# Kernel tuning notes

Hardware: AMD Instinct MI355X
Metric: run time of the kernel (lower is better)

## Reference

```python
import jax, jax.numpy as jnp
import numpy as np

# ---------------- static model configuration (mirrors NeuroNN.__init__) -------------
N = 2000
RATIO = 0.8
N_E = int(N * RATIO)
N_I = N - N_E
NMAX = 60          # Euler fixed-point steps (Nmax in Euler2fixedpt)
NAVG = 15          # trailing steps averaged for convergence metric (Navg)
DT = 1e-3
XTOL = 1e-5
XMIN = 1.0
V_THR = 20.0       # spike threshold of Ricciardi transfer fn (V_rest = 0)
SCALING_G = 1.0
W_FF = 30.0
SIG_EXT = 5.0
DEG = jnp.pi / 180.0

_IS_I = jnp.arange(N) >= N_E
PREF = jnp.concatenate([jnp.linspace(0.0, 179.99, N_E), jnp.linspace(0.0, 179.99, N_I)])
T_INV = 1.0 / jnp.where(_IS_I, 0.01 * 0.5, 0.01)          # T_E=0.01, T_I=0.005
TAU = jnp.where(_IS_I, 0.01, 0.01)                          # tau_E = tau_I = 0.01
TAU_REF = jnp.where(_IS_I, 0.001, 0.005)                    # refractory periods
# connection-type gather index: conn[i,j] = 2*(j is I) + (i is I)  -> 0:ee 1:ei 2:ie 3:ii
CONN = 2 * _IS_I[None, :].astype(jnp.int32) + _IS_I[:, None].astype(jnp.int32)
SIGN_COL = jnp.where(_IS_I, -1.0, 1.0)                      # Dale's law: sign by presynaptic column
DIFF = jnp.abs(PREF[:, None] - PREF[None, :])               # |pref_i - pref_j| (deg)

ORIENTATIONS = jnp.arange(12.0) * 15.0                       # [12]
CONTRASTS = jnp.array([0.0, 0.0432773, 0.103411, 0.186966, 0.303066, 0.464386, 0.68854, 1.0])
# circular Gaussian feed-forward drive, [12, N]
_gauss = jnp.exp((jnp.cos(2.0 * DEG * (ORIENTATIONS[:, None] - PREF[None, :])) - 1.0)
                 / (4.0 * (DEG * W_FF) ** 2))
# all 96 conditions flattened: index c*12 + o, shape [96, N]
INPUT_MEAN = (CONTRASTS[:, None, None] * 20.0 * SCALING_G * _gauss[None]).reshape(96, N)

# ------------- Ricciardi transfer function Phi (Sanzeni rational approximation) ------
_A = [0.22757881388024176, 0.77373949685442023, 0.32056016125642045,
      0.32171431660633076, 0.62718906618071668, 0.93524391761244940,
      1.0616084849547165, 0.64290613877355551, 0.14805913578876898]

def f_ricci(x):
    t = -x / (1.0 + x)
    p = jnp.zeros_like(x)
    for c in reversed(_A):      # Horner: a1*t + ... + a9*t^9
        p = p * t + c
    return jnp.log(2.0 * x + 1.0) + p * t

def g_ricci(x):
    z = x / (2.0 + x)
    enum = (3.5441754117462949 * z - 7.0529131065835378 * z**2 - 56.532378057580381 * z**3
            + 279.56761105465944 * z**4 - 520.37554793489681 * z**5
            + 456.58245777026514 * z**6 - 155.73340457809226 * z**7)
    denom = (1.0 - 4.1357968834226053 * z - 7.2984226138266743 * z**2
             + 98.656602235468327 * z**3 - 334.20436223415163 * z**4
             + 601.08633903294185 * z**5 - 599.58577549598340 * z**6
             + 277.18420330693891 * z**7 - 16.445022798669722 * z**8)
    return enum / denom

def Phi(mu, sigma, tau, tau_ref):
    xp = mu / sigma
    xm = (mu - V_THR) / sigma
    pos = xm > 0
    neg = xp <= 0
    mid = (~pos) & (~neg)
    # branch 1: 0 < xm < xp   (guard values keep unselected lanes finite for vjp)
    xps = jnp.where(pos, xp, 2.0)
    xms = jnp.where(pos, xm, 1.0)
    r_pos = 1.0 / (f_ricci(xps) - f_ricci(xms))
    # branch 2: xm <= 0 < xp
    xpm = jnp.where(mid, xp, 1.0)
    nxm = jnp.clip(jnp.where(mid, -xm, 1.0), 0.0, 9.0)
    r_mid = 1.0 / (f_ricci(xpm) + jnp.exp(nxm ** 2) * g_ricci(nxm))
    # branch 3: xm < xp <= 0
    nxp = jnp.clip(jnp.where(neg, -xp, 0.5), 0.0, 9.0)
    nxm2 = jnp.clip(jnp.where(neg, -xm, 1.0), 0.0, 9.0)
    arg = g_ricci(nxm2) - jnp.exp(nxp ** 2 - nxm2 ** 2) * g_ricci(nxp)
    r_neg = jnp.exp(-nxm2 ** 2 - jnp.log(jnp.maximum(arg, 1e-12)))
    r = jnp.where(pos, r_pos, jnp.where(mid, r_mid, r_neg))
    return 1.0 / (tau_ref + tau / jnp.maximum(r, 1e-12))

# --------------------------- weight construction ------------------------------------
def _build_weights(j_param, p_param, w_param, rand_matrix):
    J = jnp.exp(j_param)                         # positive efficacies, [4]
    P = jax.nn.sigmoid(2.0 * jnp.exp(p_param))   # probs in (0,1), steepness-2 sigmoid
    Wd = jnp.exp(w_param)                        # positive widths (deg)
    J_mat = J[CONN]                              # [N, N] gathers by connection type
    P_mat = P[CONN]
    W_mat = Wd[CONN]
    z = jnp.exp((jnp.cos(2.0 * DEG * DIFF) - 1.0) / (4.0 * (DEG * W_mat) ** 2))
    W = SIGN_COL[None, :] * J_mat * jax.nn.sigmoid(32.0 * (P_mat * z - rand_matrix))
    return W, W * W

# ------------------ Euler fixed-point solve, all 96 conditions at once ---------------
def _solve(W, W2):
    sd2 = SIG_EXT ** 2
    def step(r, _):
        mu = TAU * (r @ W.T) + INPUT_MEAN                  # [96, N]
        sig = jnp.sqrt(TAU * (r @ W2.T) + sd2)
        dr = DT * T_INV * (Phi(mu, sig, TAU, TAU_REF) - r)
        r = r + dr
        m = jnp.max(jnp.abs(dr) / jnp.maximum(jnp.abs(r), XMIN), axis=1) / XTOL  # [96]
        return r, m
    r0 = jnp.zeros((96, N), dtype=W.dtype)
    r_fp, ms = jax.lax.scan(step, r0, None, length=NMAX)
    avg_step = jnp.mean(ms[-NAVG:])
    return r_fp, avg_step

def setup_inputs() -> dict:
    key = jax.random.key(0)
    k1, k2, k3, k4 = jax.random.split(key, 4)
    j_param = jnp.log(jnp.array([2.0, 1.5, 3.0, 2.5], dtype=jnp.float32)) + 0.1 * jax.random.normal(k1, (4,), dtype=jnp.float32)
    p_param = jnp.log(jnp.array([0.4, 0.3, 0.5, 0.4], dtype=jnp.float32)) + 0.1 * jax.random.normal(k2, (4,), dtype=jnp.float32)
    w_param = jnp.log(jnp.array([32.0, 32.0, 32.0, 32.0], dtype=jnp.float32)) + 0.1 * jax.random.normal(k3, (4,), dtype=jnp.float32)
    rand_matrix = jax.random.uniform(k4, (N, N), dtype=jnp.float32)
    return {"j_param": j_param, "p_param": p_param, "w_param": w_param, "rand_matrix": rand_matrix}

def reference(j_param, p_param, w_param, rand_matrix):
    W, W2 = _build_weights(j_param, p_param, w_param, rand_matrix)
    r_fp, avg_step = _solve(W, W2)
    # [96, N] -> [8, 12, N] -> [N, contrasts, orientations] (matches permute(2,0,1))
    tuning = r_fp.reshape(8, 12, N).transpose(2, 0, 1)
    return tuning, avg_step
```

## Files before the change

### kernel.cpp

```cpp
#include <hip/hip_runtime.h>
#include <hip/hip_bf16.h>

#define N_NEUR 2000
#define N_E    1600
#define KPAD   2048
#define NCOND  96
#define NSTEP  60
#define NAVG   15
#define NBLK   250
#define RSTEP  (NCOND * KPAD)

#define DEGF   0.017453292519943295f
#define TWO_DEG 0.03490658503988659f

typedef __attribute__((ext_vector_type(8))) short bf16x8;
typedef __attribute__((ext_vector_type(4))) float f32x4;

__device__ __forceinline__ float f_ricci(float x){
    float t = -x / (1.0f + x);
    float p = 0.14805913578876898f;
    p = fmaf(p, t, 0.64290613877355551f);
    p = fmaf(p, t, 1.0616084849547165f);
    p = fmaf(p, t, 0.93524391761244940f);
    p = fmaf(p, t, 0.62718906618071668f);
    p = fmaf(p, t, 0.32171431660633076f);
    p = fmaf(p, t, 0.32056016125642045f);
    p = fmaf(p, t, 0.77373949685442023f);
    p = fmaf(p, t, 0.22757881388024176f);
    return logf(2.0f * x + 1.0f) + p * t;
}

__device__ __forceinline__ float g_ricci(float x){
    float z = x / (2.0f + x);
    float z2 = z * z, z3 = z2 * z, z4 = z2 * z2, z5 = z4 * z, z6 = z3 * z3, z7 = z6 * z, z8 = z4 * z4;
    float en = 3.5441754117462949f * z - 7.0529131065835378f * z2 - 56.532378057580381f * z3
             + 279.56761105465944f * z4 - 520.37554793489681f * z5
             + 456.58245777026514f * z6 - 155.73340457809226f * z7;
    float de = 1.0f - 4.1357968834226053f * z - 7.2984226138266743f * z2
             + 98.656602235468327f * z3 - 334.20436223415163f * z4
             + 601.08633903294185f * z5 - 599.58577549598340f * z6
             + 277.18420330693891f * z7 - 16.445022798669722f * z8;
    return en / de;
}

__device__ __forceinline__ float phi_rate(float mu, float sigma, float tau_ref){
    const float tau = 0.01f;
    float xp = mu / sigma;
    float xm = (mu - 20.0f) / sigma;
    float r;
    if (xm > 0.0f){
        r = 1.0f / (f_ricci(xp) - f_ricci(xm));
    } else if (xp > 0.0f){
        float nxm = fminf(-xm, 9.0f);
        r = 1.0f / (f_ricci(xp) + expf(nxm * nxm) * g_ricci(nxm));
    } else {
        float nxp = fminf(fmaxf(-xp, 0.0f), 9.0f);
        float nxm = fminf(-xm, 9.0f);
        float arg = g_ricci(nxm) - expf(nxp * nxp - nxm * nxm) * g_ricci(nxp);
        r = expf(-nxm * nxm - logf(fmaxf(arg, 1e-12f)));
    }
    return 1.0f / (tau_ref + tau / fmaxf(r, 1e-12f));
}

__device__ __forceinline__ float pref_of(int n){
    return (n < N_E) ? (float)n * (179.99f / 1599.0f)
                     : (float)(n - N_E) * (179.99f / 399.0f);
}

__device__ __forceinline__ unsigned short bf16_rne(float f){
    unsigned int u = __float_as_uint(f);
    u = (u + 0x7fffu + ((u >> 16) & 1u)) >> 16;
    return (unsigned short)u;
}

__device__ __forceinline__ void vmdrain(){
    asm volatile("s_waitcnt vmcnt(0)" ::: "memory");
}

__global__ __launch_bounds__(256) void build_w_kernel(
    const float* __restrict__ jp, const float* __restrict__ pp,
    const float* __restrict__ wp, const float* __restrict__ rnd,
    unsigned short* __restrict__ Wh, unsigned short* __restrict__ Wl,
    unsigned short* __restrict__ W2h)
{
    int e = blockIdx.x * 256 + threadIdx.x;
    int i = e >> 11;
    int j = e & (KPAD - 1);
    float w = 0.0f;
    if (i < N_NEUR && j < N_NEUR){
        int isIi = (i >= N_E) ? 1 : 0;
        int isIj = (j >= N_E) ? 1 : 0;
        int conn = 2 * isIj + isIi;
        float J  = expf(jp[conn]);
        float P  = 1.0f / (1.0f + expf(-2.0f * expf(pp[conn])));
        float Wd = expf(wp[conn]);
        float diff = fabsf(pref_of(i) - pref_of(j));
        float dw = DEGF * Wd;
        float z = expf((cosf(TWO_DEG * diff) - 1.0f) / (4.0f * dw * dw));
        float s = 1.0f / (1.0f + expf(-32.0f * (P * z - rnd[i * N_NEUR + j])));
        float sign = isIj ? -1.0f : 1.0f;
        w = sign * J * s;
    }
    unsigned short hb = bf16_rne(w);
    float hf = __uint_as_float(((unsigned int)hb) << 16);
    Wh[e] = hb;
    Wl[e] = bf16_rne(w - hf);
    W2h[e] = bf16_rne(w * w);
}

__global__ __launch_bounds__(256) void build_im_kernel(float* __restrict__ IM)
{
    int e = blockIdx.x * 256 + threadIdx.x;
    int c = e >> 11;
    int n = e & (KPAD - 1);
    if (n >= N_NEUR){ IM[e] = 0.0f; return; }
    const float contrasts[8] = {0.0f, 0.0432773f, 0.103411f, 0.186966f,
                                0.303066f, 0.464386f, 0.68854f, 1.0f};
    int ci = c / 12;
    int oi = c - ci * 12;
    float orient = (float)oi * 15.0f;
    const float dw = DEGF * 30.0f;
    float g = expf((cosf(TWO_DEG * (orient - pref_of(n))) - 1.0f) / (4.0f * dw * dw));
    IM[e] = contrasts[ci] * 20.0f * g;
}

__global__ __launch_bounds__(512, 2) void solve_kernel(
    const unsigned short* __restrict__ Wh, const unsigned short* __restrict__ Wl,
    const unsigned short* __restrict__ W2h,
    unsigned short* __restrict__ rh, unsigned short* __restrict__ rl,
    unsigned int* __restrict__ flags,
    const float* __restrict__ IM, float* __restrict__ out,
    float* __restrict__ mloc)
{
    __shared__ float red[8][64][25];
    __shared__ float vbuf[48][16];

    const int bid  = blockIdx.x;
    const int tile = bid >> 1;
    const int half = bid & 1;
    const int t  = threadIdx.x;
    const int wv = t >> 6;
    const int ln = t & 63;
    const int nbase = tile * 16;
    const int cbase = half * 48;

    const int lrow = ln & 15;
    const int lk8  = (ln >> 4) * 8;
    const int kw   = wv * 256 + lk8;
    const int nrow = nbase + lrow;

    const unsigned short* pwh = &Wh [nrow * KPAD + kw];
    const unsigned short* pwl = &Wl [nrow * KPAD + kw];
    const unsigned short* pw2 = &W2h[nrow * KPAD + kw];
    bf16x8 wh_f[8], wl_f[8], w2_f[8];
    #pragma unroll
    for (int s = 0; s < 8; ++s){
        wh_f[s] = *reinterpret_cast<const bf16x8*>(pwh + s * 32);
        wl_f[s] = *reinterpret_cast<const bf16x8*>(pwl + s * 32);
        w2_f[s] = *reinterpret_cast<const bf16x8*>(pw2 + s * 32);
    }

    const int wt = wv * 16 + (ln & 15);
    const bool need = (ln < 16) && (wt < 125);
    const unsigned int* fpoll = &flags[((size_t)wt * 2 + half) * 16];

    const int o0 = t, o1 = t + 512;
    const bool has1 = (o1 < 768);
    const int c_l0 = o0 >> 4, n_l0 = o0 & 15;
    const int c_l1 = o1 >> 4, n_l1 = o1 & 15;
    const int m0 = c_l0 >> 4, q0 = c_l0 & 3, lr0 = ((c_l0 & 15) >> 2) * 16 + n_l0;
    const int m1 = c_l1 >> 4, q1 = c_l1 & 3, lr1 = ((c_l1 & 15) >> 2) * 16 + n_l1;
    const int c0 = cbase + c_l0, i0n = nbase + n_l0;
    const int c1 = cbase + c_l1, i1n = nbase + n_l1;
    const float im0 = IM[c0 * KPAD + i0n];
    const float im1 = has1 ? IM[c1 * KPAD + i1n] : 0.0f;
    const bool isI0 = (i0n >= N_E), isI1 = (i1n >= N_E);
    float rf0 = 0.0f, rf1 = 0.0f;

    const int ro0 = (cbase + lrow) * KPAD + kw;

    for (int st = 0; st < NSTEP; ++st){
        if (st > 0){
            const unsigned int* fp = fpoll + (size_t)st * 256 * 16;
            for (;;){
                unsigned int v = need ? __hip_atomic_load(fp, __ATOMIC_RELAXED,
                                                          __HIP_MEMORY_SCOPE_AGENT) : 1u;
                if (__all(v != 0)) break;
                __builtin_amdgcn_s_sleep(1);
            }
        }

        const unsigned short* bhp = rh + (size_t)st * RSTEP + ro0;
        const unsigned short* blp = rl + (size_t)st * RSTEP + ro0;

        f32x4 accm[3], accs[3];
        #pragma unroll
        for (int m = 0; m < 3; ++m){
            accm[m] = (f32x4){0.0f, 0.0f, 0.0f, 0.0f};
            accs[m] = (f32x4){0.0f, 0.0f, 0.0f, 0.0f};
        }

        bf16x8 fh[3][3], fl[3][3];
        #define LOADF(b, s) do {                                                        \
            fh[b][0] = *reinterpret_cast<const bf16x8*>(bhp + (s) * 32            );    \
            fh[b][1] = *reinterpret_cast<const bf16x8*>(bhp + (s) * 32 + 16 * KPAD);    \
            fh[b][2] = *reinterpret_cast<const bf16x8*>(bhp + (s) * 32 + 32 * KPAD);    \
            fl[b][0] = *reinterpret_cast<const bf16x8*>(blp + (s) * 32            );    \
            fl[b][1] = *reinterpret_cast<const bf16x8*>(blp + (s) * 32 + 16 * KPAD);    \
            fl[b][2] = *reinterpret_cast<const bf16x8*>(blp + (s) * 32 + 32 * KPAD);    \
        } while (0)

        LOADF(0, 0);
        LOADF(1, 1);
        #pragma unroll
        for (int s = 0; s < 8; ++s){
            const int cur = s % 3;
            if (s + 2 < 8){ const int nx = (s + 2) % 3; LOADF(nx, s + 2); }
            #pragma unroll
            for (int m = 0; m < 3; ++m){
                accm[m] = __builtin_amdgcn_mfma_f32_16x16x32_bf16(fh[cur][m], wh_f[s], accm[m], 0, 0, 0);
                accm[m] = __builtin_amdgcn_mfma_f32_16x16x32_bf16(fh[cur][m], wl_f[s], accm[m], 0, 0, 0);
                accm[m] = __builtin_amdgcn_mfma_f32_16x16x32_bf16(fl[cur][m], wh_f[s], accm[m], 0, 0, 0);
                accs[m] = __builtin_amdgcn_mfma_f32_16x16x32_bf16(fh[cur][m], w2_f[s], accs[m], 0, 0, 0);
                accs[m] = __builtin_amdgcn_mfma_f32_16x16x32_bf16(fl[cur][m], w2_f[s], accs[m], 0, 0, 0);
            }
        }
        #undef LOADF

        #pragma unroll
        for (int m = 0; m < 3; ++m)
            #pragma unroll
            for (int q = 0; q < 4; ++q){
                red[wv][ln][m * 4 + q]      = accm[m][q];
                red[wv][ln][12 + m * 4 + q] = accs[m][q];
            }
        __syncthreads();

        unsigned short* rho = rh + (size_t)(st + 1) * RSTEP;
        unsigned short* rlo = rl + (size_t)(st + 1) * RSTEP;
        const bool track = (st >= NSTEP - NAVG);

        {
            float ms = 0.0f, ss = 0.0f;
            #pragma unroll
            for (int w = 0; w < 8; ++w){
                ms += red[w][lr0][m0 * 4 + q0];
                ss += red[w][lr0][12 + m0 * 4 + q0];
            }
            const float mu = fmaf(0.01f, ms, im0);
            const float sg = sqrtf(fmaf(0.01f, ss, 25.0f));
            const float rate = phi_rate(mu, sg, isI0 ? 0.001f : 0.005f);
            const float dr = (isI0 ? 0.2f : 0.1f) * (rate - rf0);
            const float rnew = rf0 + dr;
            rf0 = rnew;
            const unsigned short hb = bf16_rne(rnew);
            const float hf = __uint_as_float(((unsigned int)hb) << 16);
            __hip_atomic_store(&rho[c0 * KPAD + i0n], hb,
                               __ATOMIC_RELAXED, __HIP_MEMORY_SCOPE_AGENT);
            __hip_atomic_store(&rlo[c0 * KPAD + i0n], bf16_rne(rnew - hf),
                               __ATOMIC_RELAXED, __HIP_MEMORY_SCOPE_AGENT);
            if (track) vbuf[c_l0][n_l0] = fabsf(dr) / fmaxf(fabsf(rnew), 1.0f);
            if (st == NSTEP - 1) out[i0n * NCOND + c0] = rnew;
        }
        if (has1){
            float ms = 0.0f, ss = 0.0f;
            #pragma unroll
            for (int w = 0; w < 8; ++w){
                ms += red[w][lr1][m1 * 4 + q1];
                ss += red[w][lr1][12 + m1 * 4 + q1];
            }
            const float mu = fmaf(0.01f, ms, im1);
            const float sg = sqrtf(fmaf(0.01f, ss, 25.0f));
            const float rate = phi_rate(mu, sg, isI1 ? 0.001f : 0.005f);
            const float dr = (isI1 ? 0.2f : 0.1f) * (rate - rf1);
            const float rnew = rf1 + dr;
            rf1 = rnew;
            const unsigned short hb = bf16_rne(rnew);
            const float hf = __uint_as_float(((unsigned int)hb) << 16);
            __hip_atomic_store(&rho[c1 * KPAD + i1n], hb,
                               __ATOMIC_RELAXED, __HIP_MEMORY_SCOPE_AGENT);
            __hip_atomic_store(&rlo[c1 * KPAD + i1n], bf16_rne(rnew - hf),
                               __ATOMIC_RELAXED, __HIP_MEMORY_SCOPE_AGENT);
            if (track) vbuf[c_l1][n_l1] = fabsf(dr) / fmaxf(fabsf(rnew), 1.0f);
            if (st == NSTEP - 1) out[i1n * NCOND + c1] = rnew;
        }

        vmdrain();
        __syncthreads();
        if (st < NSTEP - 1 && t == 0)
            __hip_atomic_store(&flags[((size_t)(st + 1) * 256 + tile * 2 + half) * 16], 1u,
                               __ATOMIC_RELAXED, __HIP_MEMORY_SCOPE_AGENT);
        if (track && t < 48){
            float mx = 0.0f;
            #pragma unroll
            for (int j = 0; j < 16; ++j) mx = fmaxf(mx, vbuf[t][j]);
            mloc[((size_t)(st - (NSTEP - NAVG)) * NBLK + bid) * 48 + t] = mx;
        }
    }
}

__global__ __launch_bounds__(128) void finalize_max_kernel(
    const float* __restrict__ mloc, float* __restrict__ m2)
{
    int idx = blockIdx.x * 128 + threadIdx.x;
    if (idx >= NAVG * NCOND) return;
    int st = idx / NCOND, c = idx - st * NCOND;
    int half = c / 48, cl = c - half * 48;
    float mx = 0.0f;
    for (int tile = 0; tile < 125; ++tile)
        mx = fmaxf(mx, mloc[((size_t)st * NBLK + tile * 2 + half) * 48 + cl]);
    m2[idx] = mx;
}

__global__ __launch_bounds__(256) void finalize_sum_kernel(
    const float* __restrict__ m2, float* __restrict__ out)
{
    __shared__ float sbuf[256];
    float s = 0.0f;
    for (int i = threadIdx.x; i < NAVG * NCOND; i += 256) s += m2[i];
    sbuf[threadIdx.x] = s;
    __syncthreads();
    for (int st = 128; st > 0; st >>= 1){
        if (threadIdx.x < st) sbuf[threadIdx.x] += sbuf[threadIdx.x + st];
        __syncthreads();
    }
    if (threadIdx.x == 0)
        out[N_NEUR * NCOND] = sbuf[0] / (float)(NAVG * NCOND) * 1e5f;
}

extern "C" void kernel_launch(void* const* d_in, const int* in_sizes, int n_in,
                              void* d_out, int out_size, void* d_ws, size_t ws_size,
                              hipStream_t stream) {
    const float* jp  = (const float*)d_in[0];
    const float* pp  = (const float*)d_in[1];
    const float* wp  = (const float*)d_in[2];
    const float* rnd = (const float*)d_in[3];
    float* out = (float*)d_out;

    const size_t WELEMS = (size_t)KPAD * KPAD;
    const size_t RBUFS  = (size_t)(NSTEP + 1) * RSTEP;
    unsigned short* Wh  = (unsigned short*)d_ws;
    unsigned short* Wl  = Wh  + WELEMS;
    unsigned short* W2h = Wl  + WELEMS;
    float* IM   = (float*)(W2h + WELEMS);
    float* mloc = IM + (size_t)NCOND * KPAD;
    float* m2   = mloc + (size_t)NAVG * NBLK * 48;
    unsigned short* rh = (unsigned short*)(m2 + NAVG * NCOND);
    unsigned short* rl = rh + RBUFS;
    unsigned int* flags = (unsigned int*)(rl + RBUFS);

    hipMemsetAsync(rh, 0, (size_t)RSTEP * sizeof(unsigned short), stream);
    hipMemsetAsync(rl, 0, (size_t)RSTEP * sizeof(unsigned short), stream);
    hipMemsetAsync(flags, 0, (size_t)(NSTEP + 1) * 256 * 16 * sizeof(unsigned int), stream);

    build_w_kernel<<<(int)(WELEMS / 256), 256, 0, stream>>>(jp, pp, wp, rnd, Wh, Wl, W2h);
    build_im_kernel<<<(int)((NCOND * KPAD) / 256), 256, 0, stream>>>(IM);

    void* args[] = {(void*)&Wh, (void*)&Wl, (void*)&W2h,
                    (void*)&rh, (void*)&rl, (void*)&flags,
                    (void*)&IM, (void*)&out, (void*)&mloc};
    hipLaunchCooperativeKernel((const void*)solve_kernel, dim3(NBLK), dim3(512),
                               args, 0, stream);

    finalize_max_kernel<<<(NAVG * NCOND + 127) / 128, 128, 0, stream>>>(mloc, m2);
    finalize_sum_kernel<<<1, 256, 0, stream>>>(m2, out);
}
```

Measured before the change: 915.5 us.

## Split solver into quarter-condition blocks for twice the workgroups

The fixed-point solver now assigns each block 16 neurons by 24 conditions instead of 48, so it launches 500 blocks with a 4-per-CU launch bound and a normal launch in place of the cooperative one. This is meant to spread the per-step matvec and transfer-function work over more CUs and shorten each step's critical path. The W2 fragment is now reloaded from global every step instead of held in registers, which frees registers but adds traffic. The cross-wave reduction is now two-phase in LDS, and the second MFMA tile covers only 8 real condition rows, so half of it is wasted. The spin-wait now depends on all blocks being resident without a cooperative-launch guarantee.

```diff
diff --git a/kernel.cpp b/kernel.cpp
--- a/kernel.cpp
+++ b/kernel.cpp
@@ -7,7 +7,7 @@
 #define NCOND  96
 #define NSTEP  60
 #define NAVG   15
-#define NBLK   250
+#define NBLK   500
 #define RSTEP  (NCOND * KPAD)
 
 #define DEGF   0.017453292519943295f
@@ -124,7 +124,7 @@
     IM[e] = contrasts[ci] * 20.0f * g;
 }
 
-__global__ __launch_bounds__(512, 2) void solve_kernel(
+__global__ __launch_bounds__(512, 4) void solve_kernel(
     const unsigned short* __restrict__ Wh, const unsigned short* __restrict__ Wl,
     const unsigned short* __restrict__ W2h,
     unsigned short* __restrict__ rh, unsigned short* __restrict__ rl,
@@ -132,17 +132,17 @@
     const float* __restrict__ IM, float* __restrict__ out,
     float* __restrict__ mloc)
 {
-    __shared__ float red[8][64][25];
-    __shared__ float vbuf[48][16];
+    __shared__ float red[4][64][17];
+    __shared__ float vbuf[24][16];
 
     const int bid  = blockIdx.x;
-    const int tile = bid >> 1;
-    const int half = bid & 1;
+    const int tile = bid >> 2;
+    const int qtr  = bid & 3;
     const int t  = threadIdx.x;
     const int wv = t >> 6;
     const int ln = t & 63;
     const int nbase = tile * 16;
-    const int cbase = half * 48;
+    const int cbase = qtr * 24;
 
     const int lrow = ln & 15;
     const int lk8  = (ln >> 4) * 8;
@@ -152,36 +152,37 @@
     const unsigned short* pwh = &Wh [nrow * KPAD + kw];
     const unsigned short* pwl = &Wl [nrow * KPAD + kw];
     const unsigned short* pw2 = &W2h[nrow * KPAD + kw];
-    bf16x8 wh_f[8], wl_f[8], w2_f[8];
+    bf16x8 wh_f[8], wl_f[8];
     #pragma unroll
     for (int s = 0; s < 8; ++s){
         wh_f[s] = *reinterpret_cast<const bf16x8*>(pwh + s * 32);
         wl_f[s] = *reinterpret_cast<const bf16x8*>(pwl + s * 32);
-        w2_f[s] = *reinterpret_cast<const bf16x8*>(pw2 + s * 32);
     }
 
     const int wt = wv * 16 + (ln & 15);
     const bool need = (ln < 16) && (wt < 125);
-    const unsigned int* fpoll = &flags[((size_t)wt * 2 + half) * 16];
-
-    const int o0 = t, o1 = t + 512;
-    const bool has1 = (o1 < 768);
-    const int c_l0 = o0 >> 4, n_l0 = o0 & 15;
-    const int c_l1 = o1 >> 4, n_l1 = o1 & 15;
-    const int m0 = c_l0 >> 4, q0 = c_l0 & 3, lr0 = ((c_l0 & 15) >> 2) * 16 + n_l0;
-    const int m1 = c_l1 >> 4, q1 = c_l1 & 3, lr1 = ((c_l1 & 15) >> 2) * 16 + n_l1;
-    const int c0 = cbase + c_l0, i0n = nbase + n_l0;
-    const int c1 = cbase + c_l1, i1n = nbase + n_l1;
-    const float im0 = IM[c0 * KPAD + i0n];
-    const float im1 = has1 ? IM[c1 * KPAD + i1n] : 0.0f;
-    const bool isI0 = (i0n >= N_E), isI1 = (i1n >= N_E);
-    float rf0 = 0.0f, rf1 = 0.0f;
+    const unsigned int* fpoll = &flags[((size_t)wt * 4 + qtr) * 16];
+
+    const int c_l = t >> 4, n_l = t & 15;
+    const bool act = (t < 384);
+    const int m_e = c_l >> 4;
+    const int rr_e = c_l & 15;
+    const int q_e = rr_e & 3;
+    const int lane_e = ((rr_e >> 2) << 4) + n_l;
+    const int c_g = cbase + c_l;
+    const int i_g = nbase + n_l;
+    const float im = act ? IM[c_g * KPAD + i_g] : 0.0f;
+    const bool isI = (i_g >= N_E);
+    const float tref = isI ? 0.001f : 0.005f;
+    const float gain = isI ? 0.2f : 0.1f;
+    float rfv = 0.0f;
 
     const int ro0 = (cbase + lrow) * KPAD + kw;
+    const int ro1 = (cbase + 16 + (lrow & 7)) * KPAD + kw;
 
     for (int st = 0; st < NSTEP; ++st){
         if (st > 0){
-            const unsigned int* fp = fpoll + (size_t)st * 256 * 16;
+            const unsigned int* fp = fpoll + (size_t)st * NBLK * 16;
             for (;;){
                 unsigned int v = need ? __hip_atomic_load(fp, __ATOMIC_RELAXED,
                                                           __HIP_MEMORY_SCOPE_AGENT) : 1u;
@@ -190,111 +191,92 @@
             }
         }
 
-        const unsigned short* bhp = rh + (size_t)st * RSTEP + ro0;
-        const unsigned short* blp = rl + (size_t)st * RSTEP + ro0;
-
-        f32x4 accm[3], accs[3];
-        #pragma unroll
-        for (int m = 0; m < 3; ++m){
-            accm[m] = (f32x4){0.0f, 0.0f, 0.0f, 0.0f};
-            accs[m] = (f32x4){0.0f, 0.0f, 0.0f, 0.0f};
-        }
-
-        bf16x8 fh[3][3], fl[3][3];
-        #define LOADF(b, s) do {                                                        \
-            fh[b][0] = *reinterpret_cast<const bf16x8*>(bhp + (s) * 32            );    \
-            fh[b][1] = *reinterpret_cast<const bf16x8*>(bhp + (s) * 32 + 16 * KPAD);    \
-            fh[b][2] = *reinterpret_cast<const bf16x8*>(bhp + (s) * 32 + 32 * KPAD);    \
-            fl[b][0] = *reinterpret_cast<const bf16x8*>(blp + (s) * 32            );    \
-            fl[b][1] = *reinterpret_cast<const bf16x8*>(blp + (s) * 32 + 16 * KPAD);    \
-            fl[b][2] = *reinterpret_cast<const bf16x8*>(blp + (s) * 32 + 32 * KPAD);    \
-        } while (0)
-
-        LOADF(0, 0);
-        LOADF(1, 1);
+        const unsigned short* base_h = rh + (size_t)st * RSTEP;
+        const unsigned short* base_l = rl + (size_t)st * RSTEP;
+
+        f32x4 accm[2], accs[2];
+        accm[0] = (f32x4){0.0f, 0.0f, 0.0f, 0.0f};
+        accm[1] = (f32x4){0.0f, 0.0f, 0.0f, 0.0f};
+        accs[0] = (f32x4){0.0f, 0.0f, 0.0f, 0.0f};
+        accs[1] = (f32x4){0.0f, 0.0f, 0.0f, 0.0f};
+
         #pragma unroll
         for (int s = 0; s < 8; ++s){
-            const int cur = s % 3;
-            if (s + 2 < 8){ const int nx = (s + 2) % 3; LOADF(nx, s + 2); }
+            const bf16x8 fh0 = *reinterpret_cast<const bf16x8*>(base_h + ro0 + s * 32);
+            const bf16x8 fh1 = *reinterpret_cast<const bf16x8*>(base_h + ro1 + s * 32);
+            const bf16x8 fl0 = *reinterpret_cast<const bf16x8*>(base_l + ro0 + s * 32);
+            const bf16x8 fl1 = *reinterpret_cast<const bf16x8*>(base_l + ro1 + s * 32);
+            const bf16x8 w2s = *reinterpret_cast<const bf16x8*>(pw2 + s * 32);
+            accm[0] = __builtin_amdgcn_mfma_f32_16x16x32_bf16(fh0, wh_f[s], accm[0], 0, 0, 0);
+            accm[0] = __builtin_amdgcn_mfma_f32_16x16x32_bf16(fh0, wl_f[s], accm[0], 0, 0, 0);
+            accm[0] = __builtin_amdgcn_mfma_f32_16x16x32_bf16(fl0, wh_f[s], accm[0], 0, 0, 0);
+            accs[0] = __builtin_amdgcn_mfma_f32_16x16x32_bf16(fh0, w2s, accs[0], 0, 0, 0);
+            accs[0] = __builtin_amdgcn_mfma_f32_16x16x32_bf16(fl0, w2s, accs[0], 0, 0, 0);
+            accm[1] = __builtin_amdgcn_mfma_f32_16x16x32_bf16(fh1, wh_f[s], accm[1], 0, 0, 0);
+            accm[1] = __builtin_amdgcn_mfma_f32_16x16x32_bf16(fh1, wl_f[s], accm[1], 0, 0, 0);
+            accm[1] = __builtin_amdgcn_mfma_f32_16x16x32_bf16(fl1, wh_f[s], accm[1], 0, 0, 0);
+            accs[1] = __builtin_amdgcn_mfma_f32_16x16x32_bf16(fh1, w2s, accs[1], 0, 0, 0);
+            accs[1] = __builtin_amdgcn_mfma_f32_16x16x32_bf16(fl1, w2s, accs[1], 0, 0, 0);
+        }
+
+        if (wv >= 4){
             #pragma unroll
-            for (int m = 0; m < 3; ++m){
-                accm[m] = __builtin_amdgcn_mfma_f32_16x16x32_bf16(fh[cur][m], wh_f[s], accm[m], 0, 0, 0);
-                accm[m] = __builtin_amdgcn_mfma_f32_16x16x32_bf16(fh[cur][m], wl_f[s], accm[m], 0, 0, 0);
-                accm[m] = __builtin_amdgcn_mfma_f32_16x16x32_bf16(fl[cur][m], wh_f[s], accm[m], 0, 0, 0);
-                accs[m] = __builtin_amdgcn_mfma_f32_16x16x32_bf16(fh[cur][m], w2_f[s], accs[m], 0, 0, 0);
-                accs[m] = __builtin_amdgcn_mfma_f32_16x16x32_bf16(fl[cur][m], w2_f[s], accs[m], 0, 0, 0);
-            }
-        }
-        #undef LOADF
-
-        #pragma unroll
-        for (int m = 0; m < 3; ++m)
+            for (int m = 0; m < 2; ++m)
+                #pragma unroll
+                for (int q = 0; q < 4; ++q){
+                    red[wv - 4][ln][m * 4 + q]     = accm[m][q];
+                    red[wv - 4][ln][8 + m * 4 + q] = accs[m][q];
+                }
+        }
+        __syncthreads();
+        if (wv < 4){
             #pragma unroll
-            for (int q = 0; q < 4; ++q){
-                red[wv][ln][m * 4 + q]      = accm[m][q];
-                red[wv][ln][12 + m * 4 + q] = accs[m][q];
-            }
+            for (int m = 0; m < 2; ++m)
+                #pragma unroll
+                for (int q = 0; q < 4; ++q){
+                    red[wv][ln][m * 4 + q]     += accm[m][q];
+                    red[wv][ln][8 + m * 4 + q] += accs[m][q];
+                }
+        }
         __syncthreads();
 
         unsigned short* rho = rh + (size_t)(st + 1) * RSTEP;
         unsigned short* rlo = rl + (size_t)(st + 1) * RSTEP;
         const bool track = (st >= NSTEP - NAVG);
 
-        {
+        if (act){
             float ms = 0.0f, ss = 0.0f;
             #pragma unroll
-            for (int w = 0; w < 8; ++w){
-                ms += red[w][lr0][m0 * 4 + q0];
-                ss += red[w][lr0][12 + m0 * 4 + q0];
+            for (int w = 0; w < 4; ++w){
+                ms += red[w][lane_e][m_e * 4 + q_e];
+                ss += red[w][lane_e][8 + m_e * 4 + q_e];
             }
-            const float mu = fmaf(0.01f, ms, im0);
+            const float mu = fmaf(0.01f, ms, im);
             const float sg = sqrtf(fmaf(0.01f, ss, 25.0f));
-            const float rate = phi_rate(mu, sg, isI0 ? 0.001f : 0.005f);
-            const float dr = (isI0 ? 0.2f : 0.1f) * (rate - rf0);
-            const float rnew = rf0 + dr;
-            rf0 = rnew;
+            const float rate = phi_rate(mu, sg, tref);
+            const float dr = gain * (rate - rfv);
+            const float rnew = rfv + dr;
+            rfv = rnew;
             const unsigned short hb = bf16_rne(rnew);
             const float hf = __uint_as_float(((unsigned int)hb) << 16);
-            __hip_atomic_store(&rho[c0 * KPAD + i0n], hb,
+            __hip_atomic_store(&rho[c_g * KPAD + i_g], hb,
                                __ATOMIC_RELAXED, __HIP_MEMORY_SCOPE_AGENT);
-            __hip_atomic_store(&rlo[c0 * KPAD + i0n], bf16_rne(rnew - hf),
+            __hip_atomic_store(&rlo[c_g * KPAD + i_g], bf16_rne(rnew - hf),
                                __ATOMIC_RELAXED, __HIP_MEMORY_SCOPE_AGENT);
-            if (track) vbuf[c_l0][n_l0] = fabsf(dr) / fmaxf(fabsf(rnew), 1.0f);
-            if (st == NSTEP - 1) out[i0n * NCOND + c0] = rnew;
-        }
-        if (has1){
-            float ms = 0.0f, ss = 0.0f;
-            #pragma unroll
-            for (int w = 0; w < 8; ++w){
-                ms += red[w][lr1][m1 * 4 + q1];
-                ss += red[w][lr1][12 + m1 * 4 + q1];
-            }
-            const float mu = fmaf(0.01f, ms, im1);
-            const float sg = sqrtf(fmaf(0.01f, ss, 25.0f));
-            const float rate = phi_rate(mu, sg, isI1 ? 0.001f : 0.005f);
-            const float dr = (isI1 ? 0.2f : 0.1f) * (rate - rf1);
-            const float rnew = rf1 + dr;
-            rf1 = rnew;
-            const unsigned short hb = bf16_rne(rnew);
-            const float hf = __uint_as_float(((unsigned int)hb) << 16);
-            __hip_atomic_store(&rho[c1 * KPAD + i1n], hb,
-                               __ATOMIC_RELAXED, __HIP_MEMORY_SCOPE_AGENT);
-            __hip_atomic_store(&rlo[c1 * KPAD + i1n], bf16_rne(rnew - hf),
-                               __ATOMIC_RELAXED, __HIP_MEMORY_SCOPE_AGENT);
-            if (track) vbuf[c_l1][n_l1] = fabsf(dr) / fmaxf(fabsf(rnew), 1.0f);
-            if (st == NSTEP - 1) out[i1n * NCOND + c1] = rnew;
+            if (track) vbuf[c_l][n_l] = fabsf(dr) / fmaxf(fabsf(rnew), 1.0f);
+            if (st == NSTEP - 1) out[i_g * NCOND + c_g] = rnew;
         }
 
         vmdrain();
         __syncthreads();
         if (st < NSTEP - 1 && t == 0)
-            __hip_atomic_store(&flags[((size_t)(st + 1) * 256 + tile * 2 + half) * 16], 1u,
+            __hip_atomic_store(&flags[((size_t)(st + 1) * NBLK + tile * 4 + qtr) * 16], 1u,
                                __ATOMIC_RELAXED, __HIP_MEMORY_SCOPE_AGENT);
-        if (track && t < 48){
+        if (track && t < 24){
             float mx = 0.0f;
             #pragma unroll
             for (int j = 0; j < 16; ++j) mx = fmaxf(mx, vbuf[t][j]);
-            mloc[((size_t)(st - (NSTEP - NAVG)) * NBLK + bid) * 48 + t] = mx;
+            mloc[((size_t)(st - (NSTEP - NAVG)) * NBLK + bid) * 24 + t] = mx;
         }
     }
 }
@@ -305,10 +287,10 @@
     int idx = blockIdx.x * 128 + threadIdx.x;
     if (idx >= NAVG * NCOND) return;
     int st = idx / NCOND, c = idx - st * NCOND;
-    int half = c / 48, cl = c - half * 48;
+    int qtr = c / 24, cl = c - qtr * 24;
     float mx = 0.0f;
     for (int tile = 0; tile < 125; ++tile)
-        mx = fmaxf(mx, mloc[((size_t)st * NBLK + tile * 2 + half) * 48 + cl]);
+        mx = fmaxf(mx, mloc[((size_t)st * NBLK + tile * 4 + qtr) * 24 + cl]);
     m2[idx] = mx;
 }
 
@@ -344,23 +326,20 @@
     unsigned short* W2h = Wl  + WELEMS;
     float* IM   = (float*)(W2h + WELEMS);
     float* mloc = IM + (size_t)NCOND * KPAD;
-    float* m2   = mloc + (size_t)NAVG * NBLK * 48;
+    float* m2   = mloc + (size_t)NAVG * NBLK * 24;
     unsigned short* rh = (unsigned short*)(m2 + NAVG * NCOND);
     unsigned short* rl = rh + RBUFS;
     unsigned int* flags = (unsigned int*)(rl + RBUFS);
 
     hipMemsetAsync(rh, 0, (size_t)RSTEP * sizeof(unsigned short), stream);
     hipMemsetAsync(rl, 0, (size_t)RSTEP * sizeof(unsigned short), stream);
-    hipMemsetAsync(flags, 0, (size_t)(NSTEP + 1) * 256 * 16 * sizeof(unsigned int), stream);
+    hipMemsetAsync(flags, 0, (size_t)(NSTEP + 1) * NBLK * 16 * sizeof(unsigned int), stream);
 
     build_w_kernel<<<(int)(WELEMS / 256), 256, 0, stream>>>(jp, pp, wp, rnd, Wh, Wl, W2h);
     build_im_kernel<<<(int)((NCOND * KPAD) / 256), 256, 0, stream>>>(IM);
 
-    void* args[] = {(void*)&Wh, (void*)&Wl, (void*)&W2h,
-                    (void*)&rh, (void*)&rl, (void*)&flags,
-                    (void*)&IM, (void*)&out, (void*)&mloc};
-    hipLaunchCooperativeKernel((const void*)solve_kernel, dim3(NBLK), dim3(512),
-                               args, 0, stream);
+    solve_kernel<<<dim3(NBLK), dim3(512), 0, stream>>>(
+        Wh, Wl, W2h, rh, rl, flags, IM, out, mloc);
 
     finalize_max_kernel<<<(NAVG * NCOND + 127) / 128, 128, 0, stream>>>(mloc, m2);
     finalize_sum_kernel<<<1, 256, 0, stream>>>(m2, out);
```

Result: slower. 1.260 ms (+37.7%).
